# Performance work log

Hardware: AMD Instinct MI355X
Metric: run time of the kernel (lower is better)

## Reference

```python
import jax, jax.numpy as jnp
import numpy as np

B, NA, NT, P, DA, DM, H = 1, 4096, 1024, 32768, 128, 512, 4
DH = DA // H
DF = 4 * DA
WINDOW = 16


def _layer_norm(x, g=None, b=None, eps=1e-5):
    m = jnp.mean(x, axis=-1, keepdims=True)
    v = jnp.var(x, axis=-1, keepdims=True)
    xn = (x - m) / jnp.sqrt(v + eps)
    if g is not None:
        xn = xn * g + b
    return xn


def setup_inputs() -> dict:
    key = jax.random.key(0)
    ks = jax.random.split(key, 32)
    r = lambda k, s: (jax.random.normal(k, s, dtype=jnp.float32) * 0.05)
    return {
        'q': r(ks[0], (B, NA, DA)),
        'c_atom': r(ks[1], (B, NA, DA)),
        'h_cond': r(ks[2], (B, NT, DM)),
        'p_lm': r(ks[3], (B, P, 16)),
        't_emb': r(ks[4], (B, DA)),
        'cond_proj_w': r(ks[5], (DM, DA)), 'cond_proj_b': r(ks[6], (DA,)),
        'adaln1_w': r(ks[7], (DA, 2 * DA)), 'adaln1_b': r(ks[8], (2 * DA,)),
        'adaln2_w': r(ks[9], (DA, 2 * DA)), 'adaln2_b': r(ks[10], (2 * DA,)),
        'ln_g': jnp.ones((DA,), jnp.float32), 'ln_b': jnp.zeros((DA,), jnp.float32),
        'wq': r(ks[11], (DA, DA)), 'wk': r(ks[12], (DA, DA)),
        'wv': r(ks[13], (DA, DA)), 'wg': r(ks[14], (DA, DA)),
        'wo': r(ks[15], (DA, DA)),
        'pair_w': r(ks[16], (16, H)), 'pair_b': r(ks[17], (H,)),
        'gate1_w': r(ks[18], (DA, DA)), 'gate1_b': r(ks[19], (DA,)),
        'gate2_w': r(ks[20], (DA, DA)), 'gate2_b': r(ks[21], (DA,)),
        'sw1': r(ks[22], (DA, DF)), 'sw3': r(ks[23], (DA, DF)),
        'sw2': r(ks[24], (DF, DA)),
        'p_lm_idx': jax.random.randint(ks[25], (B, P, 2), 0, NA, dtype=jnp.int32),
        'token_idx': jnp.sort(jax.random.randint(ks[26], (B, NA), 0, NT, dtype=jnp.int32), axis=-1),
    }


def _forward(q, c_atom, h_cond, p_lm, t_emb,
             cond_proj_w, cond_proj_b, adaln1_w, adaln1_b, adaln2_w, adaln2_b,
             ln_g, ln_b, wq, wk, wv, wg, wo, pair_w, pair_b,
             gate1_w, gate1_b, gate2_w, gate2_b, sw1, sw3, sw2,
             p_lm_idx, token_idx):
    Bq, N, D = q.shape
    # gather token conditioning to atoms: (B, NA, DM)
    h_atoms = jax.vmap(lambda h, t: h[t])(h_cond, token_idx)
    cond = t_emb[:, None, :] + h_atoms @ cond_proj_w + cond_proj_b  # (B, NA, DA)
    g1, b1 = jnp.split(cond @ adaln1_w + adaln1_b, 2, axis=-1)
    q_n = (1.0 + g1) * _layer_norm(q, ln_g, ln_b) + b1

    Q = (q_n @ wq).reshape(Bq, N, H, DH)
    K = (q_n @ wk).reshape(Bq, N, H, DH)
    V = (q_n @ wv).reshape(Bq, N, H, DH)
    G_flat = q_n @ wg  # (B, N, DA); permute/reshape in torch is identity on layout

    scores = jnp.einsum('bihd,bjhd->bhij', Q, K) / jnp.sqrt(jnp.float32(DH))

    # scattered pair bias: (B, P, H) -> dense (B, H, N, N)
    bias = p_lm @ pair_w + pair_b  # (B, P, H)

    def scat(idx, bb):
        return jnp.zeros((N, N, H), bb.dtype).at[idx[:, 0], idx[:, 1]].set(bb)

    pair_bias = jax.vmap(scat)(p_lm_idx, bias).transpose(0, 3, 1, 2)
    scores = scores + pair_bias

    pos = jnp.arange(N)
    window = jnp.abs(pos[:, None] - pos[None, :]) <= WINDOW  # (N, N)
    scores = jnp.where(window[None, None, :, :], scores, -jnp.inf)

    attn = jax.nn.softmax(scores, axis=-1)
    att_out = jnp.einsum('bhij,bjhd->bihd', attn, V).reshape(Bq, N, D)

    q1 = q + jax.nn.sigmoid(G_flat) * (att_out @ wo)
    q1 = q1 + jax.nn.sigmoid(c_atom @ gate1_w + gate1_b) * q1

    g2, b2 = jnp.split(cond @ adaln2_w + adaln2_b, 2, axis=-1)
    q_n2 = (1.0 + g2) * _layer_norm(q1) + b2
    swi = (jax.nn.silu(q_n2 @ sw1) * (q_n2 @ sw3)) @ sw2
    q2 = q1 + jax.nn.sigmoid(c_atom @ gate2_w + gate2_b) * swi
    return q2  # atom_pad_mask is all-ones -> final mask multiply is identity


def reference(q, c_atom, h_cond, p_lm, t_emb,
              cond_proj_w, cond_proj_b, adaln1_w, adaln1_b, adaln2_w, adaln2_b,
              ln_g, ln_b, wq, wk, wv, wg, wo, pair_w, pair_b,
              gate1_w, gate1_b, gate2_w, gate2_b, sw1, sw3, sw2,
              p_lm_idx, token_idx):
    return _forward(q, c_atom, h_cond, p_lm, t_emb,
                    cond_proj_w, cond_proj_b, adaln1_w, adaln1_b, adaln2_w, adaln2_b,
                    ln_g, ln_b, wq, wk, wv, wg, wo, pair_w, pair_b,
                    gate1_w, gate1_b, gate2_w, gate2_b, sw1, sw3, sw2,
                    p_lm_idx, token_idx)
```

## Files before the change

### kernel.cpp

```cpp
#include <hip/hip_runtime.h>
#include <math.h>

#define NA   4096
#define DA   128
#define DM   512
#define NT   1024
#define HH   4
#define DF   512
#define PP   32768
#define WIN  16
#define BAND 33

typedef __attribute__((ext_vector_type(8))) short bf16x8;
typedef __attribute__((ext_vector_type(4))) float f32x4;

__device__ __forceinline__ float sigmoidf_(float x) { return 1.0f / (1.0f + __expf(-x)); }
__device__ __forceinline__ ushort f2bf(float f) {
    union { float f; unsigned int i; } x; x.f = f;
    unsigned int r = x.i + 0x7fffu + ((x.i >> 16) & 1u);
    return (ushort)(r >> 16);
}
__device__ __forceinline__ float bf2f(ushort u) {
    union { unsigned int i; float f; } x; x.i = ((unsigned int)u) << 16;
    return x.f;
}

__global__ __launch_bounds__(256) void k_prep(
    const float* __restrict__ hc, const float* __restrict__ ca,
    const float* __restrict__ cw, const float* __restrict__ a1, const float* __restrict__ a2,
    const float* __restrict__ wq, const float* __restrict__ wk, const float* __restrict__ wv,
    const float* __restrict__ wg, const float* __restrict__ wo,
    const float* __restrict__ g1, const float* __restrict__ g2,
    const float* __restrict__ s1, const float* __restrict__ s3, const float* __restrict__ s2,
    ushort* hcb, ushort* cab, ushort* cwT, ushort* a1T, ushort* a2T,
    ushort* wqT, ushort* wkT, ushort* wvT, ushort* wgT, ushort* woT,
    ushort* g1T, ushort* g2T, ushort* s1T, ushort* s3T, ushort* s2T,
    float* band)
{
    __shared__ float tile[32][33];
    const int y = blockIdx.y, bx = blockIdx.x, tid = threadIdx.x;
    if (y <= 1) {
        const float4* src = (const float4*)(y == 0 ? hc : ca);
        ushort* dst = y == 0 ? hcb : cab;
        for (int i = bx * 256 + tid; i < 131072; i += 16384) {
            float4 v = src[i];
            ushort4 st; st.x = f2bf(v.x); st.y = f2bf(v.y); st.z = f2bf(v.z); st.w = f2bf(v.w);
            *(ushort4*)&dst[(size_t)i * 4] = st;
        }
        return;
    }
    if (y == 15) {
        float4 z = {0.f, 0.f, 0.f, 0.f};
        float4* b4 = (float4*)band;
        for (int i = bx * 256 + tid; i < 135168; i += 16384) b4[i] = z;
        return;
    }
    const float* src; ushort* dst; int K, N;
    switch (y) {
        case 2:  src = cw; dst = cwT; K = 512; N = 128; break;
        case 3:  src = a1; dst = a1T; K = 128; N = 256; break;
        case 4:  src = a2; dst = a2T; K = 128; N = 256; break;
        case 5:  src = wq; dst = wqT; K = 128; N = 128; break;
        case 6:  src = wk; dst = wkT; K = 128; N = 128; break;
        case 7:  src = wv; dst = wvT; K = 128; N = 128; break;
        case 8:  src = wg; dst = wgT; K = 128; N = 128; break;
        case 9:  src = wo; dst = woT; K = 128; N = 128; break;
        case 10: src = g1; dst = g1T; K = 128; N = 128; break;
        case 11: src = g2; dst = g2T; K = 128; N = 128; break;
        case 12: src = s1; dst = s1T; K = 128; N = 512; break;
        case 13: src = s3; dst = s3T; K = 128; N = 512; break;
        default: src = s2; dst = s2T; K = 512; N = 128; break;
    }
    const int tn_cnt = N >> 5;
    if (bx >= (K >> 5) * tn_cnt) return;
    const int k0 = (bx / tn_cnt) << 5, n0 = (bx % tn_cnt) << 5;
    {
        int r = tid >> 3, c = (tid & 7) << 2;
        float4 v = *(const float4*)&src[(size_t)(k0 + r) * N + n0 + c];
        tile[r][c + 0] = v.x; tile[r][c + 1] = v.y;
        tile[r][c + 2] = v.z; tile[r][c + 3] = v.w;
    }
    __syncthreads();
    {
        int rn = tid >> 3, ck = (tid & 7) << 2;
        ushort4 st;
        st.x = f2bf(tile[ck + 0][rn]);
        st.y = f2bf(tile[ck + 1][rn]);
        st.z = f2bf(tile[ck + 2][rn]);
        st.w = f2bf(tile[ck + 3][rn]);
        *(ushort4*)&dst[(size_t)(n0 + rn) * K + k0 + ck] = st;
    }
}

template<int K, int NF>
__device__ __forceinline__ void gemm_core(
    const ushort* __restrict__ Arow, const ushort* __restrict__ WTcol,
    f32x4* acc, int ko)
{
    #pragma unroll
    for (int ks = 0; ks < K / 32; ++ks) {
        bf16x8 a = *(const bf16x8*)(Arow + ks * 32 + ko);
        #pragma unroll
        for (int nf = 0; nf < NF; ++nf) {
            bf16x8 b = *(const bf16x8*)(WTcol + (size_t)nf * 16 * K + ks * 32 + ko);
            acc[nf] = __builtin_amdgcn_mfma_f32_16x16x32_bf16(a, b, acc[nf], 0, 0, 0);
        }
    }
}

__global__ __launch_bounds__(256) void k_cond(
    const ushort* __restrict__ hcb, const int* __restrict__ tok,
    const ushort* __restrict__ cwT, const float* __restrict__ t_emb,
    const float* __restrict__ cond_b, ushort* __restrict__ cond_bf,
    const float* __restrict__ p_lm, const float* __restrict__ pair_w,
    const float* __restrict__ pair_b, const int* __restrict__ p_idx,
    float* __restrict__ band)
{
    const int tid = threadIdx.x, y = blockIdx.y;
    if (y >= 4) {
        int p = ((y - 4) * 64 + blockIdx.x) * 256 + tid;
        int i = p_idx[2 * p], j = p_idx[2 * p + 1];
        int d = j - i + WIN;
        if (d < 0 || d > 2 * WIN) return;
        float v0 = pair_b[0], v1 = pair_b[1], v2 = pair_b[2], v3 = pair_b[3];
        #pragma unroll
        for (int k = 0; k < 16; ++k) {
            float a = p_lm[p * 16 + k];
            v0 = fmaf(a, pair_w[k * 4 + 0], v0);
            v1 = fmaf(a, pair_w[k * 4 + 1], v1);
            v2 = fmaf(a, pair_w[k * 4 + 2], v2);
            v3 = fmaf(a, pair_w[k * 4 + 3], v3);
        }
        size_t base = ((size_t)i * HH) * BAND + d;
        band[base + 0 * BAND] = v0;
        band[base + 1 * BAND] = v1;
        band[base + 2 * BAND] = v2;
        band[base + 3 * BAND] = v3;
        return;
    }
    const int l = tid & 63, w = tid >> 6, cl = l & 15, ko = (l >> 4) * 8;
    const int m0 = blockIdx.x * 64, n0 = y * 32;
    const int trow = tok[m0 + w * 16 + cl];
    f32x4 acc[2] = {};
    gemm_core<512, 2>(hcb + (size_t)trow * DM, cwT + (size_t)(n0 + cl) * DM, acc, ko);
    const int r0 = m0 + w * 16 + (l >> 4) * 4;
    #pragma unroll
    for (int nf = 0; nf < 2; ++nf) {
        int col = n0 + nf * 16 + cl;
        float add = t_emb[col] + cond_b[col];
        #pragma unroll
        for (int r = 0; r < 4; ++r)
            cond_bf[(size_t)(r0 + r) * DA + col] = f2bf(acc[nf][r] + add);
    }
}

__global__ __launch_bounds__(256) void k_modgate(
    const ushort* __restrict__ cond_bf, const ushort* __restrict__ cab,
    const ushort* __restrict__ a1T, const ushort* __restrict__ a2T,
    const ushort* __restrict__ g1T, const ushort* __restrict__ g2T,
    const float* __restrict__ ad1b, const float* __restrict__ ad2b,
    const float* __restrict__ g1b, const float* __restrict__ g2b,
    ushort* __restrict__ gb1, ushort* __restrict__ gb2,
    ushort* __restrict__ gate1, ushort* __restrict__ gate2)
{
    const int tid = threadIdx.x, y = blockIdx.y;
    const int l = tid & 63, w = tid >> 6, cl = l & 15, ko = (l >> 4) * 8;
    const int m0 = blockIdx.x * 64;
    const int gatep = (y >= 4);
    const int n0 = gatep ? (y - 4) * 64 : y * 64;
    const ushort* A  = gatep ? cab : cond_bf;
    const ushort* W1 = gatep ? g1T : a1T;
    const ushort* W2 = gatep ? g2T : a2T;
    const float* b1 = gatep ? g1b : ad1b;
    const float* b2 = gatep ? g2b : ad2b;
    ushort* O1 = gatep ? gate1 : gb1;
    ushort* O2 = gatep ? gate2 : gb2;
    const int ldo = gatep ? DA : 256;

    const ushort* Arow = A + (size_t)(m0 + w * 16 + cl) * DA;
    const ushort* W1c = W1 + (size_t)(n0 + cl) * DA;
    const ushort* W2c = W2 + (size_t)(n0 + cl) * DA;
    f32x4 acc1[4] = {}, acc2[4] = {};
    #pragma unroll
    for (int ks = 0; ks < 4; ++ks) {
        bf16x8 a = *(const bf16x8*)(Arow + ks * 32 + ko);
        #pragma unroll
        for (int nf = 0; nf < 4; ++nf) {
            bf16x8 w1v = *(const bf16x8*)(W1c + (size_t)nf * 16 * DA + ks * 32 + ko);
            acc1[nf] = __builtin_amdgcn_mfma_f32_16x16x32_bf16(a, w1v, acc1[nf], 0, 0, 0);
            bf16x8 w2v = *(const bf16x8*)(W2c + (size_t)nf * 16 * DA + ks * 32 + ko);
            acc2[nf] = __builtin_amdgcn_mfma_f32_16x16x32_bf16(a, w2v, acc2[nf], 0, 0, 0);
        }
    }
    const int r0 = m0 + w * 16 + (l >> 4) * 4;
    #pragma unroll
    for (int nf = 0; nf < 4; ++nf) {
        int col = n0 + nf * 16 + cl;
        float bb1 = b1[col], bb2 = b2[col];
        #pragma unroll
        for (int r = 0; r < 4; ++r) {
            float v1 = acc1[nf][r] + bb1;
            float v2 = acc2[nf][r] + bb2;
            if (gatep) { v1 = sigmoidf_(v1); v2 = sigmoidf_(v2); }
            O1[(size_t)(r0 + r) * ldo + col] = f2bf(v1);
            O2[(size_t)(r0 + r) * ldo + col] = f2bf(v2);
        }
    }
}

__global__ __launch_bounds__(256) void k_ln1(
    const float* __restrict__ q, const ushort* __restrict__ gb1,
    const float* __restrict__ ln_g, const float* __restrict__ ln_b,
    ushort* __restrict__ qn_bf)
{
    const int w = threadIdx.x >> 6, l = threadIdx.x & 63;
    const int row = blockIdx.x * 4 + w;
    float2 xv = *(const float2*)&q[(size_t)row * DA + 2 * l];
    float sum = xv.x + xv.y, sq = xv.x * xv.x + xv.y * xv.y;
    #pragma unroll
    for (int off = 1; off <= 32; off <<= 1) {
        sum += __shfl_xor(sum, off);
        sq  += __shfl_xor(sq,  off);
    }
    float m = sum * (1.0f / DA);
    float rs = rsqrtf(sq * (1.0f / DA) - m * m + 1e-5f);
    ushort2 gu = *(const ushort2*)&gb1[(size_t)row * 256 + 2 * l];
    ushort2 bu = *(const ushort2*)&gb1[(size_t)row * 256 + 128 + 2 * l];
    float2 lg = *(const float2*)&ln_g[2 * l];
    float2 lb = *(const float2*)&ln_b[2 * l];
    float xn0 = (xv.x - m) * rs * lg.x + lb.x;
    float xn1 = (xv.y - m) * rs * lg.y + lb.y;
    ushort2 st;
    st.x = f2bf((1.f + bf2f(gu.x)) * xn0 + bf2f(bu.x));
    st.y = f2bf((1.f + bf2f(gu.y)) * xn1 + bf2f(bu.y));
    *(ushort2*)&qn_bf[(size_t)row * DA + 2 * l] = st;
}

__global__ __launch_bounds__(256) void k_qkvg(
    const ushort* __restrict__ qn_bf,
    const ushort* __restrict__ wqT, const ushort* __restrict__ wkT,
    const ushort* __restrict__ wvT, const ushort* __restrict__ wgT,
    float* __restrict__ Qb, float* __restrict__ Kb,
    float* __restrict__ Vb, ushort* __restrict__ sG)
{
    const int tid = threadIdx.x, l = tid & 63, w = tid >> 6;
    const int cl = l & 15, kq = l >> 4, ko = kq * 8;
    const int m0 = blockIdx.x * 64, n0 = blockIdx.y * 64, z = blockIdx.z;
    const ushort* WT = (z == 0) ? wqT : (z == 1) ? wkT : (z == 2) ? wvT : wgT;
    f32x4 acc[4] = {};
    gemm_core<128, 4>(qn_bf + (size_t)(m0 + w * 16 + cl) * DA,
                      WT + (size_t)(n0 + cl) * DA, acc, ko);
    const int r0 = m0 + w * 16 + kq * 4;
    float* O = (z == 0) ? Qb : (z == 1) ? Kb : Vb;
    #pragma unroll
    for (int nf = 0; nf < 4; ++nf) {
        int col = n0 + nf * 16 + cl;
        #pragma unroll
        for (int r = 0; r < 4; ++r) {
            size_t rc = (size_t)(r0 + r) * DA + col;
            if (z == 3) sG[rc] = f2bf(sigmoidf_(acc[nf][r]));
            else O[rc] = acc[nf][r];
        }
    }
}

__global__ __launch_bounds__(512) void k_attnwo(
    const float* __restrict__ Qb, const float* __restrict__ Kb,
    const float* __restrict__ Vb, const float* __restrict__ band,
    const float* __restrict__ q, const ushort* __restrict__ sG,
    const ushort* __restrict__ gate1, const ushort* __restrict__ woT,
    float* __restrict__ q1)
{
    __shared__ ushort att_s[16 * 128];
    const int tid = threadIdx.x;
    const int r0 = blockIdx.x * 16;
    {
        const int g = tid >> 3, l3 = tid & 7;
        const int rl = g >> 2, h = g & 3;
        const int i = r0 + rl;
        const float scale = 0.17677669529663687f;
        float4 qr = *(const float4*)(Qb + (size_t)i * DA + h * 32 + l3 * 4);
        const float* brow = band + ((size_t)i * HH + h) * BAND;
        float s[BAND];
        float m = -1e30f;
        #pragma unroll
        for (int jo = 0; jo < BAND; ++jo) {
            int j = i - WIN + jo;
            float sv = -1e30f;
            if ((unsigned)j < NA) {
                float4 kk = *(const float4*)(Kb + (size_t)j * DA + h * 32 + l3 * 4);
                float d = 0.f;
                d = fmaf(qr.x, kk.x, d); d = fmaf(qr.y, kk.y, d);
                d = fmaf(qr.z, kk.z, d); d = fmaf(qr.w, kk.w, d);
                d += __shfl_xor(d, 1);
                d += __shfl_xor(d, 2);
                d += __shfl_xor(d, 4);
                sv = fmaf(d, scale, brow[jo]);
            }
            s[jo] = sv;
            m = fmaxf(m, sv);
        }
        float lsum = 0.f;
        #pragma unroll
        for (int jo = 0; jo < BAND; ++jo) {
            float p = __expf(s[jo] - m);
            s[jo] = p;
            lsum += p;
        }
        float inv = 1.0f / lsum;
        float4 o = {0.f, 0.f, 0.f, 0.f};
        #pragma unroll
        for (int jo = 0; jo < BAND; ++jo) {
            int j = i - WIN + jo;
            if ((unsigned)j < NA) {
                float4 v = *(const float4*)(Vb + (size_t)j * DA + h * 32 + l3 * 4);
                o.x = fmaf(s[jo], v.x, o.x);
                o.y = fmaf(s[jo], v.y, o.y);
                o.z = fmaf(s[jo], v.z, o.z);
                o.w = fmaf(s[jo], v.w, o.w);
            }
        }
        ushort4 st;
        st.x = f2bf(o.x * inv); st.y = f2bf(o.y * inv);
        st.z = f2bf(o.z * inv); st.w = f2bf(o.w * inv);
        int byte = rl * 256 + h * 64 + l3 * 8;
        byte ^= (rl & 7) << 4;
        *(ushort4*)((char*)att_s + byte) = st;
    }
    __syncthreads();
    {
        const int l = tid & 63, w = tid >> 6;
        const int cl = l & 15, kq = l >> 4, ko = kq * 8;
        const int n0 = w * 16;
        f32x4 acc = {0.f, 0.f, 0.f, 0.f};
        #pragma unroll
        for (int ks = 0; ks < 4; ++ks) {
            int byteA = cl * 256 + (ks * 32 + ko) * 2;
            byteA ^= (cl & 7) << 4;
            bf16x8 a = *(const bf16x8*)((char*)att_s + byteA);
            bf16x8 b = *(const bf16x8*)(woT + (size_t)(n0 + cl) * DA + ks * 32 + ko);
            acc = __builtin_amdgcn_mfma_f32_16x16x32_bf16(a, b, acc, 0, 0, 0);
        }
        #pragma unroll
        for (int r = 0; r < 4; ++r) {
            int row = r0 + kq * 4 + r, col = n0 + cl;
            size_t rc = (size_t)row * DA + col;
            q1[rc] = (q[rc] + bf2f(sG[rc]) * acc[r]) * (1.f + bf2f(gate1[rc]));
        }
    }
}

__global__ __launch_bounds__(512) void k_ffn(
    const float* __restrict__ q1, const ushort* __restrict__ gb2,
    const ushort* __restrict__ gate2,
    const ushort* __restrict__ s1T, const ushort* __restrict__ s3T,
    const ushort* __restrict__ s2T, float* __restrict__ out)
{
    __shared__ ushort hbs[16 * 512];
    const int tid = threadIdx.x, l = tid & 63, w = tid >> 6;
    const int cl = l & 15, kq = l >> 4, ko = kq * 8;
    const int m0 = blockIdx.x * 16;
    const int row = m0 + cl;

    float qv[4][8];
    float sum = 0.f, sq = 0.f;
    #pragma unroll
    for (int ks = 0; ks < 4; ++ks) {
        float4 v0 = *(const float4*)&q1[(size_t)row * DA + ks * 32 + ko];
        float4 v1 = *(const float4*)&q1[(size_t)row * DA + ks * 32 + ko + 4];
        qv[ks][0] = v0.x; qv[ks][1] = v0.y; qv[ks][2] = v0.z; qv[ks][3] = v0.w;
        qv[ks][4] = v1.x; qv[ks][5] = v1.y; qv[ks][6] = v1.z; qv[ks][7] = v1.w;
        sum += v0.x + v0.y + v0.z + v0.w + v1.x + v1.y + v1.z + v1.w;
        sq += v0.x * v0.x + v0.y * v0.y + v0.z * v0.z + v0.w * v0.w
            + v1.x * v1.x + v1.y * v1.y + v1.z * v1.z + v1.w * v1.w;
    }
    sum += __shfl_xor(sum, 16); sq += __shfl_xor(sq, 16);
    sum += __shfl_xor(sum, 32); sq += __shfl_xor(sq, 32);
    float mean = sum * (1.0f / DA);
    float rs = rsqrtf(sq * (1.0f / DA) - mean * mean + 1e-5f);

    bf16x8 afr[4];
    #pragma unroll
    for (int ks = 0; ks < 4; ++ks) {
        int k = ks * 32 + ko;
        ushort4 g0 = *(const ushort4*)&gb2[(size_t)row * 256 + k];
        ushort4 g1v = *(const ushort4*)&gb2[(size_t)row * 256 + k + 4];
        ushort4 b0 = *(const ushort4*)&gb2[(size_t)row * 256 + 128 + k];
        ushort4 b1v = *(const ushort4*)&gb2[(size_t)row * 256 + 128 + k + 4];
        float gg[8] = {bf2f(g0.x), bf2f(g0.y), bf2f(g0.z), bf2f(g0.w),
                       bf2f(g1v.x), bf2f(g1v.y), bf2f(g1v.z), bf2f(g1v.w)};
        float bb[8] = {bf2f(b0.x), bf2f(b0.y), bf2f(b0.z), bf2f(b0.w),
                       bf2f(b1v.x), bf2f(b1v.y), bf2f(b1v.z), bf2f(b1v.w)};
        #pragma unroll
        for (int j = 0; j < 8; ++j) {
            float xn = (qv[ks][j] - mean) * rs;
            afr[ks][j] = (short)f2bf((1.f + gg[j]) * xn + bb[j]);
        }
    }

    {
        const int c0 = w * 64;
        const ushort* W1 = s1T + (size_t)(c0 + cl) * DA;
        const ushort* W3 = s3T + (size_t)(c0 + cl) * DA;
        f32x4 acc1[4] = {}, acc3[4] = {};
        #pragma unroll
        for (int ks = 0; ks < 4; ++ks) {
            #pragma unroll
            for (int nf = 0; nf < 4; ++nf) {
                bf16x8 b1 = *(const bf16x8*)(W1 + (size_t)nf * 16 * DA + ks * 32 + ko);
                acc1[nf] = __builtin_amdgcn_mfma_f32_16x16x32_bf16(afr[ks], b1, acc1[nf], 0, 0, 0);
                bf16x8 b3 = *(const bf16x8*)(W3 + (size_t)nf * 16 * DA + ks * 32 + ko);
                acc3[nf] = __builtin_amdgcn_mfma_f32_16x16x32_bf16(afr[ks], b3, acc3[nf], 0, 0, 0);
            }
        }
        #pragma unroll
        for (int nf = 0; nf < 4; ++nf) {
            #pragma unroll
            for (int r = 0; r < 4; ++r) {
                float x1 = acc1[nf][r], x3 = acc3[nf][r];
                float h = x1 * sigmoidf_(x1) * x3;
                int rr = kq * 4 + r;
                int col = c0 + nf * 16 + cl;
                int byte = rr * 1024 + col * 2;
                byte ^= (rr & 7) << 4;
                *(ushort*)((char*)hbs + byte) = f2bf(h);
            }
        }
    }
    __syncthreads();
    {
        const int n0 = w * 16;
        const ushort* W2 = s2T + (size_t)(n0 + cl) * DF;
        f32x4 acc = {0.f, 0.f, 0.f, 0.f};
        #pragma unroll
        for (int ks = 0; ks < 16; ++ks) {
            int byteA = cl * 1024 + (ks * 32 + ko) * 2;
            byteA ^= (cl & 7) << 4;
            bf16x8 a = *(const bf16x8*)((char*)hbs + byteA);
            bf16x8 b = *(const bf16x8*)(W2 + ks * 32 + ko);
            acc = __builtin_amdgcn_mfma_f32_16x16x32_bf16(a, b, acc, 0, 0, 0);
        }
        #pragma unroll
        for (int r = 0; r < 4; ++r) {
            int rowg = m0 + kq * 4 + r, col = n0 + cl;
            size_t rc = (size_t)rowg * DA + col;
            out[rc] = q1[rc] + bf2f(gate2[rc]) * acc[r];
        }
    }
}

extern "C" void kernel_launch(void* const* d_in, const int* in_sizes, int n_in,
                              void* d_out, int out_size, void* d_ws, size_t ws_size,
                              hipStream_t stream)
{
    const float* q      = (const float*)d_in[0];
    const float* c_atom = (const float*)d_in[1];
    const float* h_cond = (const float*)d_in[2];
    const float* p_lm   = (const float*)d_in[3];
    const float* t_emb  = (const float*)d_in[4];
    const float* cond_w = (const float*)d_in[5];
    const float* cond_b = (const float*)d_in[6];
    const float* ad1w   = (const float*)d_in[7];
    const float* ad1b   = (const float*)d_in[8];
    const float* ad2w   = (const float*)d_in[9];
    const float* ad2b   = (const float*)d_in[10];
    const float* ln_g   = (const float*)d_in[11];
    const float* ln_b   = (const float*)d_in[12];
    const float* wq     = (const float*)d_in[13];
    const float* wk     = (const float*)d_in[14];
    const float* wv     = (const float*)d_in[15];
    const float* wg     = (const float*)d_in[16];
    const float* wo     = (const float*)d_in[17];
    const float* pair_w = (const float*)d_in[18];
    const float* pair_b = (const float*)d_in[19];
    const float* g1w    = (const float*)d_in[20];
    const float* g1b    = (const float*)d_in[21];
    const float* g2w    = (const float*)d_in[22];
    const float* g2b    = (const float*)d_in[23];
    const float* sw1    = (const float*)d_in[24];
    const float* sw3    = (const float*)d_in[25];
    const float* sw2    = (const float*)d_in[26];
    const int*   p_idx  = (const int*)d_in[27];
    const int*   tok    = (const int*)d_in[28];
    float* out = (float*)d_out;

    size_t off = 0;
    char* base = (char*)d_ws;
    auto alloc = [&](size_t bytes) -> void* {
        void* p = base + off;
        off += (bytes + 255) & ~(size_t)255;
        return p;
    };
    ushort* hcb     = (ushort*)alloc((size_t)NT * DM * 2);
    ushort* cab     = (ushort*)alloc((size_t)NA * DA * 2);
    ushort* cwT     = (ushort*)alloc((size_t)DM * DA * 2);
    ushort* a1T     = (ushort*)alloc((size_t)256 * 128 * 2);
    ushort* a2T     = (ushort*)alloc((size_t)256 * 128 * 2);
    ushort* wqT     = (ushort*)alloc((size_t)128 * 128 * 2);
    ushort* wkT     = (ushort*)alloc((size_t)128 * 128 * 2);
    ushort* wvT     = (ushort*)alloc((size_t)128 * 128 * 2);
    ushort* wgT     = (ushort*)alloc((size_t)128 * 128 * 2);
    ushort* woT     = (ushort*)alloc((size_t)128 * 128 * 2);
    ushort* g1T     = (ushort*)alloc((size_t)128 * 128 * 2);
    ushort* g2T     = (ushort*)alloc((size_t)128 * 128 * 2);
    ushort* s1T     = (ushort*)alloc((size_t)512 * 128 * 2);
    ushort* s3T     = (ushort*)alloc((size_t)512 * 128 * 2);
    ushort* s2T     = (ushort*)alloc((size_t)128 * 512 * 2);
    ushort* cond_bf = (ushort*)alloc((size_t)NA * DA * 2);
    ushort* gb1     = (ushort*)alloc((size_t)NA * 256 * 2);
    ushort* gb2     = (ushort*)alloc((size_t)NA * 256 * 2);
    ushort* gate1   = (ushort*)alloc((size_t)NA * DA * 2);
    ushort* gate2   = (ushort*)alloc((size_t)NA * DA * 2);
    ushort* qn_bf   = (ushort*)alloc((size_t)NA * DA * 2);
    float*  Qb      = (float*)alloc((size_t)NA * DA * 4);
    float*  Kb      = (float*)alloc((size_t)NA * DA * 4);
    float*  Vb      = (float*)alloc((size_t)NA * DA * 4);
    ushort* sG      = (ushort*)alloc((size_t)NA * DA * 2);
    float*  band    = (float*)alloc((size_t)NA * HH * BAND * 4);
    float*  q1      = (float*)alloc((size_t)NA * DA * 4);

    k_prep<<<dim3(64, 16), 256, 0, stream>>>(
        h_cond, c_atom, cond_w, ad1w, ad2w, wq, wk, wv, wg, wo,
        g1w, g2w, sw1, sw3, sw2,
        hcb, cab, cwT, a1T, a2T, wqT, wkT, wvT, wgT, woT,
        g1T, g2T, s1T, s3T, s2T, band);
    k_cond<<<dim3(64, 6), 256, 0, stream>>>(hcb, tok, cwT, t_emb, cond_b, cond_bf,
                                            p_lm, pair_w, pair_b, p_idx, band);
    k_modgate<<<dim3(64, 6), 256, 0, stream>>>(cond_bf, cab, a1T, a2T, g1T, g2T,
                                               ad1b, ad2b, g1b, g2b,
                                               gb1, gb2, gate1, gate2);
    k_ln1<<<NA / 4, 256, 0, stream>>>(q, gb1, ln_g, ln_b, qn_bf);
    k_qkvg<<<dim3(64, 2, 4), 256, 0, stream>>>(qn_bf, wqT, wkT, wvT, wgT, Qb, Kb, Vb, sG);
    k_attnwo<<<NA / 16, 512, 0, stream>>>(Qb, Kb, Vb, band, q, sG, gate1, woT, q1);
    k_ffn<<<NA / 16, 512, 0, stream>>>(q1, gb2, gate2, s1T, s3T, s2T, out);
    (void)in_sizes; (void)n_in; (void)out_size; (void)ws_size;
}
```

Baseline: 186.7 us.

## Fuse cond/modgate and LN/QKVG/attention/FFN into two kernels with LDS halos

Merges the conditioning GEMM with the adaLN and gate GEMMs into one kernel, keeping cond in LDS. Also merges LN1, the QKV/G projections, banded attention, the output projection and the FFN into one mega kernel. Each block recomputes the K/V halo rows (48 rows for 16 query rows) in shared memory so that Q/K/V/sG/q1 never go through global memory. Intermediates such as gb1/gb2 and the gates now stay in fp32. The cost is redundant K/V projection work (3x), only 256 blocks of 512 threads, and high LDS use that limits occupancy.

```diff
diff --git a/kernel.cpp b/kernel.cpp
--- a/kernel.cpp
+++ b/kernel.cpp
@@ -10,6 +10,7 @@
 #define PP   32768
 #define WIN  16
 #define BAND 33
+#define KSTR 132
 
 typedef __attribute__((ext_vector_type(8))) short bf16x8;
 typedef __attribute__((ext_vector_type(4))) float f32x4;
@@ -19,10 +20,6 @@
     union { float f; unsigned int i; } x; x.f = f;
     unsigned int r = x.i + 0x7fffu + ((x.i >> 16) & 1u);
     return (ushort)(r >> 16);
-}
-__device__ __forceinline__ float bf2f(ushort u) {
-    union { unsigned int i; float f; } x; x.i = ((unsigned int)u) << 16;
-    return x.f;
 }
 
 __global__ __launch_bounds__(256) void k_prep(
@@ -92,33 +89,23 @@
     }
 }
 
-template<int K, int NF>
-__device__ __forceinline__ void gemm_core(
-    const ushort* __restrict__ Arow, const ushort* __restrict__ WTcol,
-    f32x4* acc, int ko)
-{
-    #pragma unroll
-    for (int ks = 0; ks < K / 32; ++ks) {
-        bf16x8 a = *(const bf16x8*)(Arow + ks * 32 + ko);
-        #pragma unroll
-        for (int nf = 0; nf < NF; ++nf) {
-            bf16x8 b = *(const bf16x8*)(WTcol + (size_t)nf * 16 * K + ks * 32 + ko);
-            acc[nf] = __builtin_amdgcn_mfma_f32_16x16x32_bf16(a, b, acc[nf], 0, 0, 0);
-        }
-    }
-}
-
-__global__ __launch_bounds__(256) void k_cond(
+__global__ __launch_bounds__(256) void k_condmod(
     const ushort* __restrict__ hcb, const int* __restrict__ tok,
     const ushort* __restrict__ cwT, const float* __restrict__ t_emb,
-    const float* __restrict__ cond_b, ushort* __restrict__ cond_bf,
+    const float* __restrict__ cond_b, const ushort* __restrict__ cab,
+    const ushort* __restrict__ a1T, const ushort* __restrict__ a2T,
+    const ushort* __restrict__ g1T, const ushort* __restrict__ g2T,
+    const float* __restrict__ ad1b, const float* __restrict__ ad2b,
+    const float* __restrict__ g1b, const float* __restrict__ g2b,
     const float* __restrict__ p_lm, const float* __restrict__ pair_w,
     const float* __restrict__ pair_b, const int* __restrict__ p_idx,
-    float* __restrict__ band)
+    float* __restrict__ band,
+    float* __restrict__ gb1, float* __restrict__ gb2,
+    float* __restrict__ gate1, float* __restrict__ gate2)
 {
-    const int tid = threadIdx.x, y = blockIdx.y;
-    if (y >= 4) {
-        int p = ((y - 4) * 64 + blockIdx.x) * 256 + tid;
+    const int tid = threadIdx.x, b = blockIdx.x;
+    if (b >= 256) {
+        int p = (b - 256) * 256 + tid;
         int i = p_idx[2 * p], j = p_idx[2 * p + 1];
         int d = j - i + WIN;
         if (d < 0 || d > 2 * WIN) return;
@@ -138,160 +125,214 @@
         band[base + 3 * BAND] = v3;
         return;
     }
-    const int l = tid & 63, w = tid >> 6, cl = l & 15, ko = (l >> 4) * 8;
-    const int m0 = blockIdx.x * 64, n0 = y * 32;
-    const int trow = tok[m0 + w * 16 + cl];
-    f32x4 acc[2] = {};
-    gemm_core<512, 2>(hcb + (size_t)trow * DM, cwT + (size_t)(n0 + cl) * DM, acc, ko);
-    const int r0 = m0 + w * 16 + (l >> 4) * 4;
-    #pragma unroll
-    for (int nf = 0; nf < 2; ++nf) {
-        int col = n0 + nf * 16 + cl;
-        float add = t_emb[col] + cond_b[col];
-        #pragma unroll
-        for (int r = 0; r < 4; ++r)
-            cond_bf[(size_t)(r0 + r) * DA + col] = f2bf(acc[nf][r] + add);
+    __shared__ ushort cond_s[16 * 128];
+    const int l = tid & 63, wv = tid >> 6;
+    const int cl = l & 15, kq = l >> 4, ko = kq * 8;
+    const int r0 = b * 16;
+    {
+        const int n0 = wv * 32;
+        const ushort* Arow = hcb + (size_t)tok[r0 + cl] * DM;
+        const ushort* Wc = cwT + (size_t)(n0 + cl) * DM;
+        f32x4 acc[2] = {};
+        #pragma unroll
+        for (int ks = 0; ks < 16; ++ks) {
+            bf16x8 a = *(const bf16x8*)(Arow + ks * 32 + ko);
+            #pragma unroll
+            for (int nf = 0; nf < 2; ++nf) {
+                bf16x8 bb = *(const bf16x8*)(Wc + (size_t)nf * 16 * DM + ks * 32 + ko);
+                acc[nf] = __builtin_amdgcn_mfma_f32_16x16x32_bf16(a, bb, acc[nf], 0, 0, 0);
+            }
+        }
+        #pragma unroll
+        for (int nf = 0; nf < 2; ++nf) {
+            int col = n0 + nf * 16 + cl;
+            float add = t_emb[col] + cond_b[col];
+            #pragma unroll
+            for (int r = 0; r < 4; ++r) {
+                int row = kq * 4 + r;
+                int byte = row * 256 + col * 2;
+                byte ^= (row & 7) << 4;
+                *(ushort*)((char*)cond_s + byte) = f2bf(acc[nf][r] + add);
+            }
+        }
+    }
+    __syncthreads();
+    {
+        const int n0 = wv * 64;
+        const ushort* W1c = a1T + (size_t)(n0 + cl) * DA;
+        const ushort* W2c = a2T + (size_t)(n0 + cl) * DA;
+        f32x4 acc1[4] = {}, acc2[4] = {};
+        #pragma unroll
+        for (int ks = 0; ks < 4; ++ks) {
+            int byteA = cl * 256 + (ks * 32 + ko) * 2;
+            byteA ^= (cl & 7) << 4;
+            bf16x8 a = *(const bf16x8*)((char*)cond_s + byteA);
+            #pragma unroll
+            for (int nf = 0; nf < 4; ++nf) {
+                bf16x8 b1 = *(const bf16x8*)(W1c + (size_t)nf * 16 * DA + ks * 32 + ko);
+                acc1[nf] = __builtin_amdgcn_mfma_f32_16x16x32_bf16(a, b1, acc1[nf], 0, 0, 0);
+                bf16x8 b2 = *(const bf16x8*)(W2c + (size_t)nf * 16 * DA + ks * 32 + ko);
+                acc2[nf] = __builtin_amdgcn_mfma_f32_16x16x32_bf16(a, b2, acc2[nf], 0, 0, 0);
+            }
+        }
+        #pragma unroll
+        for (int nf = 0; nf < 4; ++nf) {
+            int col = n0 + nf * 16 + cl;
+            float b1v = ad1b[col], b2v = ad2b[col];
+            #pragma unroll
+            for (int r = 0; r < 4; ++r) {
+                size_t rc = (size_t)(r0 + kq * 4 + r) * 256 + col;
+                gb1[rc] = acc1[nf][r] + b1v;
+                gb2[rc] = acc2[nf][r] + b2v;
+            }
+        }
+    }
+    {
+        const int n0 = wv * 32;
+        const ushort* Arow = cab + (size_t)(r0 + cl) * DA;
+        const ushort* W1c = g1T + (size_t)(n0 + cl) * DA;
+        const ushort* W2c = g2T + (size_t)(n0 + cl) * DA;
+        f32x4 acc1[2] = {}, acc2[2] = {};
+        #pragma unroll
+        for (int ks = 0; ks < 4; ++ks) {
+            bf16x8 a = *(const bf16x8*)(Arow + ks * 32 + ko);
+            #pragma unroll
+            for (int nf = 0; nf < 2; ++nf) {
+                bf16x8 b1 = *(const bf16x8*)(W1c + (size_t)nf * 16 * DA + ks * 32 + ko);
+                acc1[nf] = __builtin_amdgcn_mfma_f32_16x16x32_bf16(a, b1, acc1[nf], 0, 0, 0);
+                bf16x8 b2 = *(const bf16x8*)(W2c + (size_t)nf * 16 * DA + ks * 32 + ko);
+                acc2[nf] = __builtin_amdgcn_mfma_f32_16x16x32_bf16(a, b2, acc2[nf], 0, 0, 0);
+            }
+        }
+        #pragma unroll
+        for (int nf = 0; nf < 2; ++nf) {
+            int col = n0 + nf * 16 + cl;
+            float b1v = g1b[col], b2v = g2b[col];
+            #pragma unroll
+            for (int r = 0; r < 4; ++r) {
+                size_t rc = (size_t)(r0 + kq * 4 + r) * DA + col;
+                gate1[rc] = sigmoidf_(acc1[nf][r] + b1v);
+                gate2[rc] = sigmoidf_(acc2[nf][r] + b2v);
+            }
+        }
     }
 }
 
-__global__ __launch_bounds__(256) void k_modgate(
-    const ushort* __restrict__ cond_bf, const ushort* __restrict__ cab,
-    const ushort* __restrict__ a1T, const ushort* __restrict__ a2T,
-    const ushort* __restrict__ g1T, const ushort* __restrict__ g2T,
-    const float* __restrict__ ad1b, const float* __restrict__ ad2b,
-    const float* __restrict__ g1b, const float* __restrict__ g2b,
-    ushort* __restrict__ gb1, ushort* __restrict__ gb2,
-    ushort* __restrict__ gate1, ushort* __restrict__ gate2)
-{
-    const int tid = threadIdx.x, y = blockIdx.y;
-    const int l = tid & 63, w = tid >> 6, cl = l & 15, ko = (l >> 4) * 8;
-    const int m0 = blockIdx.x * 64;
-    const int gatep = (y >= 4);
-    const int n0 = gatep ? (y - 4) * 64 : y * 64;
-    const ushort* A  = gatep ? cab : cond_bf;
-    const ushort* W1 = gatep ? g1T : a1T;
-    const ushort* W2 = gatep ? g2T : a2T;
-    const float* b1 = gatep ? g1b : ad1b;
-    const float* b2 = gatep ? g2b : ad2b;
-    ushort* O1 = gatep ? gate1 : gb1;
-    ushort* O2 = gatep ? gate2 : gb2;
-    const int ldo = gatep ? DA : 256;
-
-    const ushort* Arow = A + (size_t)(m0 + w * 16 + cl) * DA;
-    const ushort* W1c = W1 + (size_t)(n0 + cl) * DA;
-    const ushort* W2c = W2 + (size_t)(n0 + cl) * DA;
-    f32x4 acc1[4] = {}, acc2[4] = {};
-    #pragma unroll
-    for (int ks = 0; ks < 4; ++ks) {
-        bf16x8 a = *(const bf16x8*)(Arow + ks * 32 + ko);
-        #pragma unroll
-        for (int nf = 0; nf < 4; ++nf) {
-            bf16x8 w1v = *(const bf16x8*)(W1c + (size_t)nf * 16 * DA + ks * 32 + ko);
-            acc1[nf] = __builtin_amdgcn_mfma_f32_16x16x32_bf16(a, w1v, acc1[nf], 0, 0, 0);
-            bf16x8 w2v = *(const bf16x8*)(W2c + (size_t)nf * 16 * DA + ks * 32 + ko);
-            acc2[nf] = __builtin_amdgcn_mfma_f32_16x16x32_bf16(a, w2v, acc2[nf], 0, 0, 0);
-        }
-    }
-    const int r0 = m0 + w * 16 + (l >> 4) * 4;
-    #pragma unroll
-    for (int nf = 0; nf < 4; ++nf) {
-        int col = n0 + nf * 16 + cl;
-        float bb1 = b1[col], bb2 = b2[col];
-        #pragma unroll
-        for (int r = 0; r < 4; ++r) {
-            float v1 = acc1[nf][r] + bb1;
-            float v2 = acc2[nf][r] + bb2;
-            if (gatep) { v1 = sigmoidf_(v1); v2 = sigmoidf_(v2); }
-            O1[(size_t)(r0 + r) * ldo + col] = f2bf(v1);
-            O2[(size_t)(r0 + r) * ldo + col] = f2bf(v2);
-        }
-    }
-}
-
-__global__ __launch_bounds__(256) void k_ln1(
-    const float* __restrict__ q, const ushort* __restrict__ gb1,
-    const float* __restrict__ ln_g, const float* __restrict__ ln_b,
-    ushort* __restrict__ qn_bf)
-{
-    const int w = threadIdx.x >> 6, l = threadIdx.x & 63;
-    const int row = blockIdx.x * 4 + w;
-    float2 xv = *(const float2*)&q[(size_t)row * DA + 2 * l];
-    float sum = xv.x + xv.y, sq = xv.x * xv.x + xv.y * xv.y;
-    #pragma unroll
-    for (int off = 1; off <= 32; off <<= 1) {
-        sum += __shfl_xor(sum, off);
-        sq  += __shfl_xor(sq,  off);
-    }
-    float m = sum * (1.0f / DA);
-    float rs = rsqrtf(sq * (1.0f / DA) - m * m + 1e-5f);
-    ushort2 gu = *(const ushort2*)&gb1[(size_t)row * 256 + 2 * l];
-    ushort2 bu = *(const ushort2*)&gb1[(size_t)row * 256 + 128 + 2 * l];
-    float2 lg = *(const float2*)&ln_g[2 * l];
-    float2 lb = *(const float2*)&ln_b[2 * l];
-    float xn0 = (xv.x - m) * rs * lg.x + lb.x;
-    float xn1 = (xv.y - m) * rs * lg.y + lb.y;
-    ushort2 st;
-    st.x = f2bf((1.f + bf2f(gu.x)) * xn0 + bf2f(bu.x));
-    st.y = f2bf((1.f + bf2f(gu.y)) * xn1 + bf2f(bu.y));
-    *(ushort2*)&qn_bf[(size_t)row * DA + 2 * l] = st;
-}
-
-__global__ __launch_bounds__(256) void k_qkvg(
-    const ushort* __restrict__ qn_bf,
+__global__ __launch_bounds__(512) void k_mega(
+    const float* __restrict__ qg, const float* __restrict__ gb1,
+    const float* __restrict__ gb2, const float* __restrict__ gate1,
+    const float* __restrict__ gate2, const float* __restrict__ ln_g,
+    const float* __restrict__ ln_b, const float* __restrict__ band,
     const ushort* __restrict__ wqT, const ushort* __restrict__ wkT,
     const ushort* __restrict__ wvT, const ushort* __restrict__ wgT,
-    float* __restrict__ Qb, float* __restrict__ Kb,
-    float* __restrict__ Vb, ushort* __restrict__ sG)
+    const ushort* __restrict__ woT, const ushort* __restrict__ s1T,
+    const ushort* __restrict__ s3T, const ushort* __restrict__ s2T,
+    float* __restrict__ out)
 {
-    const int tid = threadIdx.x, l = tid & 63, w = tid >> 6;
+    __shared__ ushort qn_s[48 * 128];
+    __shared__ float  K_s[48 * KSTR];
+    __shared__ float  V_s[48 * KSTR];
+    __shared__ float  Q_s[16 * KSTR];
+    __shared__ float  sG_s[16 * KSTR];
+    __shared__ float  q1_s[16 * KSTR];
+    __shared__ ushort att_s[16 * 128];
+    __shared__ ushort hb_s[16 * 512];
+
+    const int tid = threadIdx.x;
+    const int l = tid & 63, wv = tid >> 6;
     const int cl = l & 15, kq = l >> 4, ko = kq * 8;
-    const int m0 = blockIdx.x * 64, n0 = blockIdx.y * 64, z = blockIdx.z;
-    const ushort* WT = (z == 0) ? wqT : (z == 1) ? wkT : (z == 2) ? wvT : wgT;
-    f32x4 acc[4] = {};
-    gemm_core<128, 4>(qn_bf + (size_t)(m0 + w * 16 + cl) * DA,
-                      WT + (size_t)(n0 + cl) * DA, acc, ko);
-    const int r0 = m0 + w * 16 + kq * 4;
-    float* O = (z == 0) ? Qb : (z == 1) ? Kb : Vb;
+    const int r0 = blockIdx.x * 16;
+    const int hb0 = r0 - 16;
+
     #pragma unroll
-    for (int nf = 0; nf < 4; ++nf) {
-        int col = n0 + nf * 16 + cl;
-        #pragma unroll
-        for (int r = 0; r < 4; ++r) {
-            size_t rc = (size_t)(r0 + r) * DA + col;
-            if (z == 3) sG[rc] = f2bf(sigmoidf_(acc[nf][r]));
-            else O[rc] = acc[nf][r];
-        }
-    }
-}
-
-__global__ __launch_bounds__(512) void k_attnwo(
-    const float* __restrict__ Qb, const float* __restrict__ Kb,
-    const float* __restrict__ Vb, const float* __restrict__ band,
-    const float* __restrict__ q, const ushort* __restrict__ sG,
-    const ushort* __restrict__ gate1, const ushort* __restrict__ woT,
-    float* __restrict__ q1)
-{
-    __shared__ ushort att_s[16 * 128];
-    const int tid = threadIdx.x;
-    const int r0 = blockIdx.x * 16;
+    for (int rr = 0; rr < 6; ++rr) {
+        int hr = wv * 6 + rr;
+        int gr = hb0 + hr;
+        ushort2 st = {0, 0};
+        if ((unsigned)gr < NA) {
+            float2 xv = *(const float2*)&qg[(size_t)gr * DA + 2 * l];
+            float sum = xv.x + xv.y, sq = xv.x * xv.x + xv.y * xv.y;
+            #pragma unroll
+            for (int off = 1; off <= 32; off <<= 1) {
+                sum += __shfl_xor(sum, off);
+                sq  += __shfl_xor(sq,  off);
+            }
+            float m = sum * (1.0f / DA);
+            float rs = rsqrtf(sq * (1.0f / DA) - m * m + 1e-5f);
+            float2 g = *(const float2*)&gb1[(size_t)gr * 256 + 2 * l];
+            float2 bb = *(const float2*)&gb1[(size_t)gr * 256 + 128 + 2 * l];
+            float2 lg = *(const float2*)&ln_g[2 * l];
+            float2 lb = *(const float2*)&ln_b[2 * l];
+            float xn0 = (xv.x - m) * rs * lg.x + lb.x;
+            float xn1 = (xv.y - m) * rs * lg.y + lb.y;
+            st.x = f2bf((1.f + g.x) * xn0 + bb.x);
+            st.y = f2bf((1.f + g.y) * xn1 + bb.y);
+        }
+        int byte = hr * 256 + 4 * l;
+        byte ^= (hr & 7) << 4;
+        *(ushort2*)((char*)qn_s + byte) = st;
+    }
+    __syncthreads();
+
+    {
+        int t, isV = 0;
+        const ushort* WT;
+        if (wv < 6) { t = wv >> 1; isV = wv & 1; WT = isV ? wvT : wkT; }
+        else        { t = 1; WT = (wv == 6) ? wqT : wgT; }
+        const ushort* Wc = WT + (size_t)cl * DA;
+        f32x4 acc[8] = {};
+        #pragma unroll
+        for (int ks = 0; ks < 4; ++ks) {
+            int byteA = (t * 16 + cl) * 256 + (ks * 32 + ko) * 2;
+            byteA ^= (cl & 7) << 4;
+            bf16x8 a = *(const bf16x8*)((char*)qn_s + byteA);
+            #pragma unroll
+            for (int nf = 0; nf < 8; ++nf) {
+                bf16x8 b = *(const bf16x8*)(Wc + (size_t)nf * 16 * DA + ks * 32 + ko);
+                acc[nf] = __builtin_amdgcn_mfma_f32_16x16x32_bf16(a, b, acc[nf], 0, 0, 0);
+            }
+        }
+        if (wv < 6) {
+            float* dst = isV ? V_s : K_s;
+            #pragma unroll
+            for (int nf = 0; nf < 8; ++nf)
+                #pragma unroll
+                for (int r = 0; r < 4; ++r)
+                    dst[(t * 16 + kq * 4 + r) * KSTR + nf * 16 + cl] = acc[nf][r];
+        } else if (wv == 6) {
+            #pragma unroll
+            for (int nf = 0; nf < 8; ++nf)
+                #pragma unroll
+                for (int r = 0; r < 4; ++r)
+                    Q_s[(kq * 4 + r) * KSTR + nf * 16 + cl] = acc[nf][r];
+        } else {
+            #pragma unroll
+            for (int nf = 0; nf < 8; ++nf)
+                #pragma unroll
+                for (int r = 0; r < 4; ++r)
+                    sG_s[(kq * 4 + r) * KSTR + nf * 16 + cl] = sigmoidf_(acc[nf][r]);
+        }
+    }
+    __syncthreads();
+
     {
         const int g = tid >> 3, l3 = tid & 7;
         const int rl = g >> 2, h = g & 3;
-        const int i = r0 + rl;
+        const int gr = r0 + rl;
         const float scale = 0.17677669529663687f;
-        float4 qr = *(const float4*)(Qb + (size_t)i * DA + h * 32 + l3 * 4);
-        const float* brow = band + ((size_t)i * HH + h) * BAND;
+        float4 qr0 = *(const float4*)&Q_s[rl * KSTR + h * 32 + l3 * 4];
+        const float* brow = band + ((size_t)gr * HH + h) * BAND;
         float s[BAND];
         float m = -1e30f;
         #pragma unroll
         for (int jo = 0; jo < BAND; ++jo) {
-            int j = i - WIN + jo;
+            int j = gr - WIN + jo;
             float sv = -1e30f;
             if ((unsigned)j < NA) {
-                float4 kk = *(const float4*)(Kb + (size_t)j * DA + h * 32 + l3 * 4);
+                float4 kk = *(const float4*)&K_s[(rl + jo) * KSTR + h * 32 + l3 * 4];
                 float d = 0.f;
-                d = fmaf(qr.x, kk.x, d); d = fmaf(qr.y, kk.y, d);
-                d = fmaf(qr.z, kk.z, d); d = fmaf(qr.w, kk.w, d);
+                d = fmaf(qr0.x, kk.x, d); d = fmaf(qr0.y, kk.y, d);
+                d = fmaf(qr0.z, kk.z, d); d = fmaf(qr0.w, kk.w, d);
                 d += __shfl_xor(d, 1);
                 d += __shfl_xor(d, 2);
                 d += __shfl_xor(d, 4);
@@ -311,9 +352,9 @@
         float4 o = {0.f, 0.f, 0.f, 0.f};
         #pragma unroll
         for (int jo = 0; jo < BAND; ++jo) {
-            int j = i - WIN + jo;
+            int j = gr - WIN + jo;
             if ((unsigned)j < NA) {
-                float4 v = *(const float4*)(Vb + (size_t)j * DA + h * 32 + l3 * 4);
+                float4 v = *(const float4*)&V_s[(rl + jo) * KSTR + h * 32 + l3 * 4];
                 o.x = fmaf(s[jo], v.x, o.x);
                 o.y = fmaf(s[jo], v.y, o.y);
                 o.z = fmaf(s[jo], v.z, o.z);
@@ -328,78 +369,69 @@
         *(ushort4*)((char*)att_s + byte) = st;
     }
     __syncthreads();
-    {
-        const int l = tid & 63, w = tid >> 6;
-        const int cl = l & 15, kq = l >> 4, ko = kq * 8;
-        const int n0 = w * 16;
+
+    {
+        const int n0 = wv * 16;
+        const ushort* Wc = woT + (size_t)(n0 + cl) * DA;
         f32x4 acc = {0.f, 0.f, 0.f, 0.f};
         #pragma unroll
         for (int ks = 0; ks < 4; ++ks) {
             int byteA = cl * 256 + (ks * 32 + ko) * 2;
             byteA ^= (cl & 7) << 4;
             bf16x8 a = *(const bf16x8*)((char*)att_s + byteA);
-            bf16x8 b = *(const bf16x8*)(woT + (size_t)(n0 + cl) * DA + ks * 32 + ko);
+            bf16x8 b = *(const bf16x8*)(Wc + ks * 32 + ko);
             acc = __builtin_amdgcn_mfma_f32_16x16x32_bf16(a, b, acc, 0, 0, 0);
         }
         #pragma unroll
         for (int r = 0; r < 4; ++r) {
-            int row = r0 + kq * 4 + r, col = n0 + cl;
-            size_t rc = (size_t)row * DA + col;
-            q1[rc] = (q[rc] + bf2f(sG[rc]) * acc[r]) * (1.f + bf2f(gate1[rc]));
-        }
-    }
-}
-
-__global__ __launch_bounds__(512) void k_ffn(
-    const float* __restrict__ q1, const ushort* __restrict__ gb2,
-    const ushort* __restrict__ gate2,
-    const ushort* __restrict__ s1T, const ushort* __restrict__ s3T,
-    const ushort* __restrict__ s2T, float* __restrict__ out)
-{
-    __shared__ ushort hbs[16 * 512];
-    const int tid = threadIdx.x, l = tid & 63, w = tid >> 6;
-    const int cl = l & 15, kq = l >> 4, ko = kq * 8;
-    const int m0 = blockIdx.x * 16;
-    const int row = m0 + cl;
-
-    float qv[4][8];
-    float sum = 0.f, sq = 0.f;
-    #pragma unroll
-    for (int ks = 0; ks < 4; ++ks) {
-        float4 v0 = *(const float4*)&q1[(size_t)row * DA + ks * 32 + ko];
-        float4 v1 = *(const float4*)&q1[(size_t)row * DA + ks * 32 + ko + 4];
-        qv[ks][0] = v0.x; qv[ks][1] = v0.y; qv[ks][2] = v0.z; qv[ks][3] = v0.w;
-        qv[ks][4] = v1.x; qv[ks][5] = v1.y; qv[ks][6] = v1.z; qv[ks][7] = v1.w;
-        sum += v0.x + v0.y + v0.z + v0.w + v1.x + v1.y + v1.z + v1.w;
-        sq += v0.x * v0.x + v0.y * v0.y + v0.z * v0.z + v0.w * v0.w
-            + v1.x * v1.x + v1.y * v1.y + v1.z * v1.z + v1.w * v1.w;
-    }
-    sum += __shfl_xor(sum, 16); sq += __shfl_xor(sq, 16);
-    sum += __shfl_xor(sum, 32); sq += __shfl_xor(sq, 32);
-    float mean = sum * (1.0f / DA);
-    float rs = rsqrtf(sq * (1.0f / DA) - mean * mean + 1e-5f);
+            int row = kq * 4 + r;
+            int gr = r0 + row, col = n0 + cl;
+            float qv = qg[(size_t)gr * DA + col];
+            float sg = sG_s[row * KSTR + col];
+            float g1v = gate1[(size_t)gr * DA + col];
+            q1_s[row * KSTR + col] = (qv + sg * acc[r]) * (1.f + g1v);
+        }
+    }
+    __syncthreads();
 
     bf16x8 afr[4];
-    #pragma unroll
-    for (int ks = 0; ks < 4; ++ks) {
-        int k = ks * 32 + ko;
-        ushort4 g0 = *(const ushort4*)&gb2[(size_t)row * 256 + k];
-        ushort4 g1v = *(const ushort4*)&gb2[(size_t)row * 256 + k + 4];
-        ushort4 b0 = *(const ushort4*)&gb2[(size_t)row * 256 + 128 + k];
-        ushort4 b1v = *(const ushort4*)&gb2[(size_t)row * 256 + 128 + k + 4];
-        float gg[8] = {bf2f(g0.x), bf2f(g0.y), bf2f(g0.z), bf2f(g0.w),
-                       bf2f(g1v.x), bf2f(g1v.y), bf2f(g1v.z), bf2f(g1v.w)};
-        float bb[8] = {bf2f(b0.x), bf2f(b0.y), bf2f(b0.z), bf2f(b0.w),
-                       bf2f(b1v.x), bf2f(b1v.y), bf2f(b1v.z), bf2f(b1v.w)};
-        #pragma unroll
-        for (int j = 0; j < 8; ++j) {
-            float xn = (qv[ks][j] - mean) * rs;
-            afr[ks][j] = (short)f2bf((1.f + gg[j]) * xn + bb[j]);
-        }
-    }
-
-    {
-        const int c0 = w * 64;
+    {
+        const int row = cl, gr = r0 + cl;
+        float qv2[4][8];
+        float sum = 0.f, sq = 0.f;
+        #pragma unroll
+        for (int ks = 0; ks < 4; ++ks) {
+            float4 v0 = *(const float4*)&q1_s[row * KSTR + ks * 32 + ko];
+            float4 v1 = *(const float4*)&q1_s[row * KSTR + ks * 32 + ko + 4];
+            qv2[ks][0] = v0.x; qv2[ks][1] = v0.y; qv2[ks][2] = v0.z; qv2[ks][3] = v0.w;
+            qv2[ks][4] = v1.x; qv2[ks][5] = v1.y; qv2[ks][6] = v1.z; qv2[ks][7] = v1.w;
+            sum += v0.x + v0.y + v0.z + v0.w + v1.x + v1.y + v1.z + v1.w;
+            sq += v0.x * v0.x + v0.y * v0.y + v0.z * v0.z + v0.w * v0.w
+                + v1.x * v1.x + v1.y * v1.y + v1.z * v1.z + v1.w * v1.w;
+        }
+        sum += __shfl_xor(sum, 16); sq += __shfl_xor(sq, 16);
+        sum += __shfl_xor(sum, 32); sq += __shfl_xor(sq, 32);
+        float mean = sum * (1.0f / DA);
+        float rs = rsqrtf(sq * (1.0f / DA) - mean * mean + 1e-5f);
+        #pragma unroll
+        for (int ks = 0; ks < 4; ++ks) {
+            int k = ks * 32 + ko;
+            float4 g0 = *(const float4*)&gb2[(size_t)gr * 256 + k];
+            float4 g1v = *(const float4*)&gb2[(size_t)gr * 256 + k + 4];
+            float4 b0 = *(const float4*)&gb2[(size_t)gr * 256 + 128 + k];
+            float4 b1v = *(const float4*)&gb2[(size_t)gr * 256 + 128 + k + 4];
+            float gg[8] = {g0.x, g0.y, g0.z, g0.w, g1v.x, g1v.y, g1v.z, g1v.w};
+            float bb[8] = {b0.x, b0.y, b0.z, b0.w, b1v.x, b1v.y, b1v.z, b1v.w};
+            #pragma unroll
+            for (int j = 0; j < 8; ++j) {
+                float xn = (qv2[ks][j] - mean) * rs;
+                afr[ks][j] = (short)f2bf((1.f + gg[j]) * xn + bb[j]);
+            }
+        }
+    }
+
+    {
+        const int c0 = wv * 64;
         const ushort* W1 = s1T + (size_t)(c0 + cl) * DA;
         const ushort* W3 = s3T + (size_t)(c0 + cl) * DA;
         f32x4 acc1[4] = {}, acc3[4] = {};
@@ -423,28 +455,29 @@
                 int col = c0 + nf * 16 + cl;
                 int byte = rr * 1024 + col * 2;
                 byte ^= (rr & 7) << 4;
-                *(ushort*)((char*)hbs + byte) = f2bf(h);
-            }
-        }
-    }
-    __syncthreads();
-    {
-        const int n0 = w * 16;
+                *(ushort*)((char*)hb_s + byte) = f2bf(h);
+            }
+        }
+    }
+    __syncthreads();
+    {
+        const int n0 = wv * 16;
         const ushort* W2 = s2T + (size_t)(n0 + cl) * DF;
         f32x4 acc = {0.f, 0.f, 0.f, 0.f};
         #pragma unroll
         for (int ks = 0; ks < 16; ++ks) {
             int byteA = cl * 1024 + (ks * 32 + ko) * 2;
             byteA ^= (cl & 7) << 4;
-            bf16x8 a = *(const bf16x8*)((char*)hbs + byteA);
+            bf16x8 a = *(const bf16x8*)((char*)hb_s + byteA);
             bf16x8 b = *(const bf16x8*)(W2 + ks * 32 + ko);
             acc = __builtin_amdgcn_mfma_f32_16x16x32_bf16(a, b, acc, 0, 0, 0);
         }
         #pragma unroll
         for (int r = 0; r < 4; ++r) {
-            int rowg = m0 + kq * 4 + r, col = n0 + cl;
-            size_t rc = (size_t)rowg * DA + col;
-            out[rc] = q1[rc] + bf2f(gate2[rc]) * acc[r];
+            int row = kq * 4 + r;
+            int gr = r0 + row, col = n0 + cl;
+            size_t rc = (size_t)gr * DA + col;
+            out[rc] = q1_s[row * KSTR + col] + gate2[rc] * acc[r];
         }
     }
 }
@@ -506,32 +539,24 @@
     ushort* s1T     = (ushort*)alloc((size_t)512 * 128 * 2);
     ushort* s3T     = (ushort*)alloc((size_t)512 * 128 * 2);
     ushort* s2T     = (ushort*)alloc((size_t)128 * 512 * 2);
-    ushort* cond_bf = (ushort*)alloc((size_t)NA * DA * 2);
-    ushort* gb1     = (ushort*)alloc((size_t)NA * 256 * 2);
-    ushort* gb2     = (ushort*)alloc((size_t)NA * 256 * 2);
-    ushort* gate1   = (ushort*)alloc((size_t)NA * DA * 2);
-    ushort* gate2   = (ushort*)alloc((size_t)NA * DA * 2);
-    ushort* qn_bf   = (ushort*)alloc((size_t)NA * DA * 2);
-    float*  Qb      = (float*)alloc((size_t)NA * DA * 4);
-    float*  Kb      = (float*)alloc((size_t)NA * DA * 4);
-    float*  Vb      = (float*)alloc((size_t)NA * DA * 4);
-    ushort* sG      = (ushort*)alloc((size_t)NA * DA * 2);
+    float*  gb1     = (float*)alloc((size_t)NA * 256 * 4);
+    float*  gb2     = (float*)alloc((size_t)NA * 256 * 4);
+    float*  gate1   = (float*)alloc((size_t)NA * DA * 4);
+    float*  gate2   = (float*)alloc((size_t)NA * DA * 4);
     float*  band    = (float*)alloc((size_t)NA * HH * BAND * 4);
-    float*  q1      = (float*)alloc((size_t)NA * DA * 4);
 
     k_prep<<<dim3(64, 16), 256, 0, stream>>>(
         h_cond, c_atom, cond_w, ad1w, ad2w, wq, wk, wv, wg, wo,
         g1w, g2w, sw1, sw3, sw2,
         hcb, cab, cwT, a1T, a2T, wqT, wkT, wvT, wgT, woT,
         g1T, g2T, s1T, s3T, s2T, band);
-    k_cond<<<dim3(64, 6), 256, 0, stream>>>(hcb, tok, cwT, t_emb, cond_b, cond_bf,
-                                            p_lm, pair_w, pair_b, p_idx, band);
-    k_modgate<<<dim3(64, 6), 256, 0, stream>>>(cond_bf, cab, a1T, a2T, g1T, g2T,
-                                               ad1b, ad2b, g1b, g2b,
-                                               gb1, gb2, gate1, gate2);
-    k_ln1<<<NA / 4, 256, 0, stream>>>(q, gb1, ln_g, ln_b, qn_bf);
-    k_qkvg<<<dim3(64, 2, 4), 256, 0, stream>>>(qn_bf, wqT, wkT, wvT, wgT, Qb, Kb, Vb, sG);
-    k_attnwo<<<NA / 16, 512, 0, stream>>>(Qb, Kb, Vb, band, q, sG, gate1, woT, q1);
-    k_ffn<<<NA / 16, 512, 0, stream>>>(q1, gb2, gate2, s1T, s3T, s2T, out);
+    k_condmod<<<384, 256, 0, stream>>>(
+        hcb, tok, cwT, t_emb, cond_b, cab,
+        a1T, a2T, g1T, g2T, ad1b, ad2b, g1b, g2b,
+        p_lm, pair_w, pair_b, p_idx, band,
+        gb1, gb2, gate1, gate2);
+    k_mega<<<256, 512, 0, stream>>>(
+        q, gb1, gb2, gate1, gate2, ln_g, ln_b, band,
+        wqT, wkT, wvT, wgT, woT, s1T, s3T, s2T, out);
     (void)in_sizes; (void)n_in; (void)out_size; (void)ws_size;
 }
```

Measured after the change: 168.5 us. 9.7% less time.
